# Optimization experiments

Hardware: AMD Instinct MI355X
Metric: run time of the kernel (lower is better)

## Reference

```python
import jax, jax.numpy as jnp
import numpy as np

B, N, C, H = 32, 577, 768, 12

def setup_inputs() -> dict:
    key = jax.random.key(0)
    k1, k2, k3, k4 = jax.random.split(key, 4)
    x = jax.random.normal(k1, (B, N, C), dtype=jnp.float32)
    prev = jax.random.normal(k2, (B, H, N, N), dtype=jnp.float32)
    Wqkv = jax.random.normal(k3, (3 * C, C), dtype=jnp.float32) * (C ** -0.5)
    Wproj = jax.random.normal(k4, (C, C), dtype=jnp.float32) * (C ** -0.5)
    bproj = jnp.zeros((C,), dtype=jnp.float32)
    return {"x": x, "prev": prev, "Wqkv": Wqkv, "Wproj": Wproj, "bproj": bproj}

def reference(x, prev, Wqkv, Wproj, bproj):
    b, n, c = x.shape
    h = H
    hd = c // h
    scale = hd ** -0.5
    # qkv: [B, N, 3C] -> [3, B, H, N, hd]
    qkv = (x @ Wqkv.T).reshape(b, n, 3, h, hd).transpose(2, 0, 3, 1, 4)
    q, k, v = qkv[0], qkv[1], qkv[2]
    # pre-softmax scores with residual passthrough (res_score=True)
    scores = jnp.einsum('bhqd,bhkd->bhqk', q, k) * scale + prev
    attn = jax.nn.softmax(scores, axis=-1)
    out = jnp.einsum('bhqk,bhkd->bhqd', attn, v)  # [B, H, N, hd]
    out = out.transpose(0, 2, 1, 3).reshape(b, n, c)
    out = out @ Wproj.T + bproj
    return out, scores
```

## Files before the change

### kernel.cpp

```cpp
#include <hip/hip_runtime.h>
#include <cstdint>
#include <cstddef>

using short8   = __attribute__((ext_vector_type(8))) short;
using f32x4    = __attribute__((ext_vector_type(4))) float;
using ushort4v = __attribute__((ext_vector_type(4))) unsigned short;

#define B_    32
#define N_    577
#define C_    768
#define H_    12
#define HD_   64
#define NPAD  640
#define MROWS 18464
#define MPAD  18560
#define NQKV  2304
#define SCALE 0.125f
#define OUT0_ELTS 14180352

static __device__ __forceinline__ unsigned short f2bf(float f) {
  union { float f; unsigned int u; } v; v.f = f;
  return (unsigned short)((v.u + 0x7FFFu + ((v.u >> 16) & 1u)) >> 16);
}

static __device__ __forceinline__ void gload_lds16(const unsigned short* g, unsigned short* l) {
  __builtin_amdgcn_global_load_lds(
      (const __attribute__((address_space(1))) unsigned int*)g,
      (__attribute__((address_space(3))) unsigned int*)l, 16, 0, 0);
}

__global__ __launch_bounds__(256) void cvt_f32_bf16(const float* __restrict__ src,
                                                    unsigned short* __restrict__ dst, int n4) {
  int i = blockIdx.x * 256 + threadIdx.x;
  if (i >= n4) return;
  f32x4 v = ((const f32x4*)src)[i];
  ushort4v o;
  o.x = f2bf(v.x); o.y = f2bf(v.y); o.z = f2bf(v.z); o.w = f2bf(v.w);
  ((ushort4v*)dst)[i] = o;
}

__global__ __launch_bounds__(256) void gemm_qkv(
    const unsigned short* __restrict__ A,
    const unsigned short* __restrict__ Bw,
    unsigned short* __restrict__ qb,
    unsigned short* __restrict__ kbuf,
    unsigned short* __restrict__ vtb)
{
  __shared__ unsigned short As[128 * 64];
  __shared__ unsigned short Bs[128 * 64];
  const int mt = blockIdx.x, nt = blockIdx.y;
  const int tid = threadIdx.x;
  const int wave = tid >> 6, lane = tid & 63;
  const int wm = wave >> 1, wn = wave & 1;
  const int lq = lane & 15, grp = lane >> 4;

  f32x4 acc[4][4] = {};

  const int arowbase = mt * 128;
  const int browbase = nt * 128;
  const int srow = wave * 8 + (lane >> 3);
  const int scol = (lane & 7) * 8;

  for (int kblk = 0; kblk < 12; ++kblk) {
    const int koff = kblk * 64;
#pragma unroll
    for (int i = 0; i < 4; ++i) {
      gload_lds16(A  + (size_t)(arowbase + i * 32 + srow) * 768 + koff + scol,
                  &As[(i * 32 + wave * 8) * 64]);
      gload_lds16(Bw + (size_t)(browbase + i * 32 + srow) * 768 + koff + scol,
                  &Bs[(i * 32 + wave * 8) * 64]);
    }
    __syncthreads();
#pragma unroll
    for (int ks = 0; ks < 2; ++ks) {
      short8 af[4], bf[4];
#pragma unroll
      for (int mi = 0; mi < 4; ++mi)
        af[mi] = *(const short8*)&As[(wm * 64 + mi * 16 + lq) * 64 + ks * 32 + grp * 8];
#pragma unroll
      for (int ni = 0; ni < 4; ++ni)
        bf[ni] = *(const short8*)&Bs[(wn * 64 + ni * 16 + lq) * 64 + ks * 32 + grp * 8];
#pragma unroll
      for (int mi = 0; mi < 4; ++mi)
#pragma unroll
        for (int ni = 0; ni < 4; ++ni)
          acc[mi][ni] = __builtin_amdgcn_mfma_f32_16x16x32_bf16(af[mi], bf[ni], acc[mi][ni], 0, 0, 0);
    }
    __syncthreads();
  }

#pragma unroll
  for (int mi = 0; mi < 4; ++mi) {
#pragma unroll
    for (int ni = 0; ni < 4; ++ni) {
      const int n = browbase + wn * 64 + ni * 16 + lq;
      const unsigned s = (unsigned)n / 768u;
      const int rem = n - (int)s * 768;
      const int hh = rem >> 6, d = rem & 63;
#pragma unroll
      for (int j = 0; j < 4; ++j) {
        const int m = arowbase + wm * 64 + mi * 16 + grp * 4 + j;
        if (m < MROWS) {
          const unsigned bb = (unsigned)m / 577u;
          const int t = m - (int)bb * 577;
          const unsigned short bv = f2bf(acc[mi][ni][j]);
          const size_t bh = (size_t)bb * H_ + hh;
          if (s == 0)      qb  [(bh * NPAD + t) * HD_ + d] = bv;
          else if (s == 1) kbuf[(bh * NPAD + t) * HD_ + d] = bv;
          else             vtb [(bh * HD_ + d) * NPAD + t] = bv;
        }
      }
    }
  }
}

__global__ __launch_bounds__(256, 3) void attn_kernel(
    const unsigned short* __restrict__ qb,
    const unsigned short* __restrict__ kb,
    const unsigned short* __restrict__ vtb,
    const float* __restrict__ prev,
    float* __restrict__ scores_out,
    unsigned short* __restrict__ ob)
{
  const int qblk = blockIdx.x;
  const int bh   = blockIdx.y;
  const int wave = threadIdx.x >> 6;
  const int lane = threadIdx.x & 63;
  const int lq = lane & 15, grp = lane >> 4;

  const int b = bh / H_;
  const int h = bh - b * H_;

  const unsigned short* qp = qb  + (size_t)bh * NPAD * HD_;
  const unsigned short* kp = kb  + (size_t)bh * NPAD * HD_;
  const unsigned short* vp = vtb + (size_t)bh * HD_ * NPAD;

  const int qrow = qblk * 64 + wave * 16 + lq;
  const bool qvalid = (qrow < N_);

  const float* prevrow = prev + ((size_t)bh * N_ + qrow) * N_;
  float* srow = scores_out + ((size_t)bh * N_ + qrow) * N_;

  short8 qf0, qf1;
  {
    const unsigned short* qr = qp + (size_t)qrow * HD_ + grp * 8;
    qf0 = *(const short8*)(qr);
    qf1 = *(const short8*)(qr + 32);
  }

  f32x4 oacc[4] = {};
  float lacc = 0.f;

  __shared__ __attribute__((aligned(16))) unsigned short plds[2][4][16][72];

  auto loadK = [&](int kblk, short8 kf[8]) {
#pragma unroll
    for (int t = 0; t < 4; ++t) {
      const unsigned short* kr = kp + (size_t)(kblk * 64 + t * 16 + lq) * HD_ + grp * 8;
      kf[2 * t]     = *(const short8*)(kr);
      kf[2 * t + 1] = *(const short8*)(kr + 32);
    }
  };
  auto loadPrev = [&](int kblk, float pv[16]) {
#pragma unroll
    for (int t = 0; t < 4; ++t) {
      const int kg0 = kblk * 64 + t * 16 + grp * 4;
      float tmp[4] = {0.f, 0.f, 0.f, 0.f};
      if (qvalid) {
        if (kg0 + 3 < N_) {
          __builtin_memcpy(tmp, prevrow + kg0, 16);
        } else {
#pragma unroll
          for (int e = 0; e < 4; ++e)
            if (kg0 + e < N_) tmp[e] = prevrow[kg0 + e];
        }
      }
#pragma unroll
      for (int e = 0; e < 4; ++e) pv[t * 4 + e] = tmp[e];
    }
  };

  short8 kf[8];
  float  pv[16];
  loadK(0, kf);
  loadPrev(0, pv);

  for (int kblk = 0; kblk < 10; ++kblk) {
    const int kbase = kblk * 64;

    short8 vf[8];
#pragma unroll
    for (int dt = 0; dt < 4; ++dt) {
      const unsigned short* vr = vp + (size_t)(dt * 16 + lq) * NPAD + kbase + grp * 8;
      vf[2 * dt]     = *(const short8*)(vr);
      vf[2 * dt + 1] = *(const short8*)(vr + 32);
    }

    float pvn[16];
    if (kblk < 9) loadPrev(kblk + 1, pvn);

    f32x4 sacc[4] = {};
#pragma unroll
    for (int t = 0; t < 4; ++t) {
      sacc[t] = __builtin_amdgcn_mfma_f32_16x16x32_bf16(kf[2 * t],     qf0, sacc[t], 0, 0, 0);
      sacc[t] = __builtin_amdgcn_mfma_f32_16x16x32_bf16(kf[2 * t + 1], qf1, sacc[t], 0, 0, 0);
    }

    short8 kfn[8];
    if (kblk < 9) loadK(kblk + 1, kfn);

    float p[16];
#pragma unroll
    for (int t = 0; t < 4; ++t) {
      const int kg0 = kbase + t * 16 + grp * 4;
      float sv[4];
#pragma unroll
      for (int r = 0; r < 4; ++r) {
        float sval = sacc[t][r] * SCALE + pv[t * 4 + r];
        if (kg0 + r >= N_) sval = -__builtin_inff();
        sv[r] = sval;
        float e = __expf(sval);
        p[t * 4 + r] = e;
        lacc += e;
      }
      if (qvalid) {
        if (kg0 + 3 < N_) {
          __builtin_memcpy(srow + kg0, sv, 16);
        } else {
#pragma unroll
          for (int e2 = 0; e2 < 4; ++e2)
            if (kg0 + e2 < N_) srow[kg0 + e2] = sv[e2];
        }
      }
    }

    const int pb = kblk & 1;
#pragma unroll
    for (int t = 0; t < 4; ++t) {
      ushort4v pw;
      pw.x = f2bf(p[t * 4 + 0]); pw.y = f2bf(p[t * 4 + 1]);
      pw.z = f2bf(p[t * 4 + 2]); pw.w = f2bf(p[t * 4 + 3]);
      *(ushort4v*)(&plds[pb][wave][lq][t * 16 + grp * 4]) = pw;
    }
    short8 pf0 = *(const short8*)(&plds[pb][wave][lq][grp * 8]);
    short8 pf1 = *(const short8*)(&plds[pb][wave][lq][32 + grp * 8]);

#pragma unroll
    for (int dt = 0; dt < 4; ++dt) {
      oacc[dt] = __builtin_amdgcn_mfma_f32_16x16x32_bf16(vf[2 * dt],     pf0, oacc[dt], 0, 0, 0);
      oacc[dt] = __builtin_amdgcn_mfma_f32_16x16x32_bf16(vf[2 * dt + 1], pf1, oacc[dt], 0, 0, 0);
    }

    if (kblk < 9) {
#pragma unroll
      for (int i = 0; i < 16; ++i) pv[i] = pvn[i];
#pragma unroll
      for (int i = 0; i < 8; ++i) kf[i] = kfn[i];
    }
  }

  lacc += __shfl_xor(lacc, 16, 64);
  lacc += __shfl_xor(lacc, 32, 64);

  if (qvalid) {
    const float rl = 1.0f / lacc;
    unsigned short* orow = ob + (size_t)(b * N_ + qrow) * C_ + h * HD_;
#pragma unroll
    for (int dt = 0; dt < 4; ++dt) {
      ushort4v ow;
      ow.x = f2bf(oacc[dt][0] * rl); ow.y = f2bf(oacc[dt][1] * rl);
      ow.z = f2bf(oacc[dt][2] * rl); ow.w = f2bf(oacc[dt][3] * rl);
      *(ushort4v*)(orow + dt * 16 + grp * 4) = ow;
    }
  }
}

__global__ __launch_bounds__(256) void gemm_proj(
    const unsigned short* __restrict__ A,
    const unsigned short* __restrict__ Bw,
    const float* __restrict__ bias,
    float* __restrict__ out0)
{
  __shared__ unsigned short As[128 * 64];
  __shared__ unsigned short Bs[128 * 64];
  const int mt = blockIdx.x, nt = blockIdx.y;
  const int tid = threadIdx.x;
  const int wave = tid >> 6, lane = tid & 63;
  const int wm = wave >> 1, wn = wave & 1;
  const int lq = lane & 15, grp = lane >> 4;

  f32x4 acc[4][4] = {};

  const int arowbase = mt * 128;
  const int browbase = nt * 128;
  const int srow = wave * 8 + (lane >> 3);
  const int scol = (lane & 7) * 8;

  for (int kblk = 0; kblk < 12; ++kblk) {
    const int koff = kblk * 64;
#pragma unroll
    for (int i = 0; i < 4; ++i) {
      gload_lds16(A  + (size_t)(arowbase + i * 32 + srow) * 768 + koff + scol,
                  &As[(i * 32 + wave * 8) * 64]);
      gload_lds16(Bw + (size_t)(browbase + i * 32 + srow) * 768 + koff + scol,
                  &Bs[(i * 32 + wave * 8) * 64]);
    }
    __syncthreads();
#pragma unroll
    for (int ks = 0; ks < 2; ++ks) {
      short8 af[4], bf[4];
#pragma unroll
      for (int mi = 0; mi < 4; ++mi)
        af[mi] = *(const short8*)&As[(wm * 64 + mi * 16 + lq) * 64 + ks * 32 + grp * 8];
#pragma unroll
      for (int ni = 0; ni < 4; ++ni)
        bf[ni] = *(const short8*)&Bs[(wn * 64 + ni * 16 + lq) * 64 + ks * 32 + grp * 8];
#pragma unroll
      for (int mi = 0; mi < 4; ++mi)
#pragma unroll
        for (int ni = 0; ni < 4; ++ni)
          acc[mi][ni] = __builtin_amdgcn_mfma_f32_16x16x32_bf16(af[mi], bf[ni], acc[mi][ni], 0, 0, 0);
    }
    __syncthreads();
  }

#pragma unroll
  for (int ni = 0; ni < 4; ++ni) {
    const int n = browbase + wn * 64 + ni * 16 + lq;
    const float bv = bias[n];
#pragma unroll
    for (int mi = 0; mi < 4; ++mi) {
#pragma unroll
      for (int j = 0; j < 4; ++j) {
        const int m = arowbase + wm * 64 + mi * 16 + grp * 4 + j;
        if (m < MROWS) out0[(size_t)m * C_ + n] = acc[mi][ni][j] + bv;
      }
    }
  }
}

extern "C" void kernel_launch(void* const* d_in, const int* in_sizes, int n_in,
                              void* d_out, int out_size, void* d_ws, size_t ws_size,
                              hipStream_t stream) {
  const float* x     = (const float*)d_in[0];
  const float* prev  = (const float*)d_in[1];
  const float* Wqkv  = (const float*)d_in[2];
  const float* Wproj = (const float*)d_in[3];
  const float* bproj = (const float*)d_in[4];
  float* out = (float*)d_out;

  char* ws = (char*)d_ws;
  size_t off = 0;
  auto alloc = [&](size_t bytes) {
    void* p = ws + off;
    off += (bytes + 255) & ~(size_t)255;
    return p;
  };
  unsigned short* xb     = (unsigned short*)alloc((size_t)MPAD * 768 * 2);
  unsigned short* wqkvb  = (unsigned short*)alloc((size_t)NQKV * 768 * 2);
  unsigned short* wprojb = (unsigned short*)alloc((size_t)768 * 768 * 2);
  unsigned short* qb     = (unsigned short*)alloc((size_t)B_ * H_ * NPAD * HD_ * 2);
  unsigned short* kbuf   = (unsigned short*)alloc((size_t)B_ * H_ * NPAD * HD_ * 2);
  unsigned short* vtb    = (unsigned short*)alloc((size_t)B_ * H_ * HD_ * NPAD * 2);
  unsigned short* ob     = (unsigned short*)alloc((size_t)MPAD * 768 * 2);
  (void)ob;

  hipMemsetAsync(vtb, 0, (size_t)B_ * H_ * HD_ * NPAD * 2, stream);

  {
    int n4 = (B_ * N_ * C_) / 4;
    cvt_f32_bf16<<<(n4 + 255) / 256, 256, 0, stream>>>(x, xb, n4);
    n4 = (NQKV * C_) / 4;
    cvt_f32_bf16<<<(n4 + 255) / 256, 256, 0, stream>>>(Wqkv, wqkvb, n4);
    n4 = (C_ * C_) / 4;
    cvt_f32_bf16<<<(n4 + 255) / 256, 256, 0, stream>>>(Wproj, wprojb, n4);
  }

  gemm_qkv<<<dim3(MPAD / 128, NQKV / 128), 256, 0, stream>>>(xb, wqkvb, qb, kbuf, vtb);

  attn_kernel<<<dim3(10, B_ * H_), 256, 0, stream>>>(qb, kbuf, vtb, prev,
                                                     out + OUT0_ELTS, ob);

  gemm_proj<<<dim3(MPAD / 128, C_ / 128), 256, 0, stream>>>(ob, wprojb, bproj, out);
}
```

Measured before the change: 714.3 us.

## Stage K/V tiles in LDS and coalesce score stores via shared slab

Each K and V tile is now loaded once per block into double-buffered shared memory using direct global-to-LDS loads with an XOR swizzle, instead of every wave fetching its own copy into registers. Scores are written to an LDS slab and read back row-contiguous, so the fp32 score output goes out in coalesced 64-wide row segments. The same slab also rebuilds the P operand layout for the second MFMA, replacing the old bf16 P shuffle buffer. This adds a block-wide barrier per key block and more LDS use, which may reduce occupancy.

```diff
diff --git a/kernel.cpp b/kernel.cpp
--- a/kernel.cpp
+++ b/kernel.cpp
@@ -124,8 +124,9 @@
 {
   const int qblk = blockIdx.x;
   const int bh   = blockIdx.y;
-  const int wave = threadIdx.x >> 6;
-  const int lane = threadIdx.x & 63;
+  const int tid  = threadIdx.x;
+  const int wave = tid >> 6;
+  const int lane = tid & 63;
   const int lq = lane & 15, grp = lane >> 4;
 
   const int b = bh / H_;
@@ -139,7 +140,11 @@
   const bool qvalid = (qrow < N_);
 
   const float* prevrow = prev + ((size_t)bh * N_ + qrow) * N_;
-  float* srow = scores_out + ((size_t)bh * N_ + qrow) * N_;
+  float* srow_base = scores_out + (size_t)bh * N_ * N_;
+
+  __shared__ __attribute__((aligned(16))) unsigned short ldsK[2][4096];
+  __shared__ __attribute__((aligned(16))) unsigned short ldsV[2][4096];
+  __shared__ __attribute__((aligned(16))) float sslab[4][16][68];
 
   short8 qf0, qf1;
   {
@@ -151,16 +156,19 @@
   f32x4 oacc[4] = {};
   float lacc = 0.f;
 
-  __shared__ __attribute__((aligned(16))) unsigned short plds[2][4][16][72];
-
-  auto loadK = [&](int kblk, short8 kf[8]) {
-#pragma unroll
-    for (int t = 0; t < 4; ++t) {
-      const unsigned short* kr = kp + (size_t)(kblk * 64 + t * 16 + lq) * HD_ + grp * 8;
-      kf[2 * t]     = *(const short8*)(kr);
-      kf[2 * t + 1] = *(const short8*)(kr + 32);
+  const int rhi = tid >> 3;
+  const int chk = (tid & 7) ^ (rhi & 7);
+  auto stageKV = [&](int kblk, int bufi) {
+    const int kbase = kblk * 64;
+#pragma unroll
+    for (int r = 0; r < 2; ++r) {
+      gload_lds16(kp + (size_t)(kbase + r * 32 + rhi) * HD_ + chk * 8,
+                  &ldsK[bufi][r * 2048 + wave * 512]);
+      gload_lds16(vp + (size_t)(r * 32 + rhi) * NPAD + kbase + chk * 8,
+                  &ldsV[bufi][r * 2048 + wave * 512]);
     }
   };
+
   auto loadPrev = [&](int kblk, float pv[16]) {
 #pragma unroll
     for (int t = 0; t < 4; ++t) {
@@ -180,82 +188,108 @@
     }
   };
 
-  short8 kf[8];
-  float  pv[16];
-  loadK(0, kf);
+  const int sl0 = ((grp)     ^ (lq & 7)) * 8;
+  const int sl1 = ((grp + 4) ^ (lq & 7)) * 8;
+
+  float pv[16], pvn[16];
+  stageKV(0, 0);
   loadPrev(0, pv);
 
+#pragma unroll 1
   for (int kblk = 0; kblk < 10; ++kblk) {
+    __syncthreads();
+    const int cur = kblk & 1;
     const int kbase = kblk * 64;
 
-    short8 vf[8];
-#pragma unroll
-    for (int dt = 0; dt < 4; ++dt) {
-      const unsigned short* vr = vp + (size_t)(dt * 16 + lq) * NPAD + kbase + grp * 8;
-      vf[2 * dt]     = *(const short8*)(vr);
-      vf[2 * dt + 1] = *(const short8*)(vr + 32);
-    }
-
-    float pvn[16];
-    if (kblk < 9) loadPrev(kblk + 1, pvn);
+    if (kblk < 9) {
+      stageKV(kblk + 1, cur ^ 1);
+      loadPrev(kblk + 1, pvn);
+    }
 
     f32x4 sacc[4] = {};
 #pragma unroll
     for (int t = 0; t < 4; ++t) {
-      sacc[t] = __builtin_amdgcn_mfma_f32_16x16x32_bf16(kf[2 * t],     qf0, sacc[t], 0, 0, 0);
-      sacc[t] = __builtin_amdgcn_mfma_f32_16x16x32_bf16(kf[2 * t + 1], qf1, sacc[t], 0, 0, 0);
-    }
-
-    short8 kfn[8];
-    if (kblk < 9) loadK(kblk + 1, kfn);
-
-    float p[16];
+      const int row = (t * 16 + lq) * 64;
+      short8 a0 = *(const short8*)&ldsK[cur][row + sl0];
+      short8 a1 = *(const short8*)&ldsK[cur][row + sl1];
+      sacc[t] = __builtin_amdgcn_mfma_f32_16x16x32_bf16(a0, qf0, sacc[t], 0, 0, 0);
+      sacc[t] = __builtin_amdgcn_mfma_f32_16x16x32_bf16(a1, qf1, sacc[t], 0, 0, 0);
+    }
+
 #pragma unroll
     for (int t = 0; t < 4; ++t) {
       const int kg0 = kbase + t * 16 + grp * 4;
-      float sv[4];
+      f32x4 sv;
 #pragma unroll
       for (int r = 0; r < 4; ++r) {
         float sval = sacc[t][r] * SCALE + pv[t * 4 + r];
         if (kg0 + r >= N_) sval = -__builtin_inff();
         sv[r] = sval;
-        float e = __expf(sval);
-        p[t * 4 + r] = e;
-        lacc += e;
-      }
-      if (qvalid) {
-        if (kg0 + 3 < N_) {
-          __builtin_memcpy(srow + kg0, sv, 16);
+      }
+      *(f32x4*)&sslab[wave][lq][t * 16 + grp * 4] = sv;
+    }
+
+    short8 pf0, pf1;
+    {
+      const float* sr = &sslab[wave][lq][0];
+      f32x4 x0 = *(const f32x4*)(sr + grp * 8);
+      f32x4 x1 = *(const f32x4*)(sr + grp * 8 + 4);
+      f32x4 x2 = *(const f32x4*)(sr + 32 + grp * 8);
+      f32x4 x3 = *(const f32x4*)(sr + 32 + grp * 8 + 4);
+      float e[16];
+#pragma unroll
+      for (int j = 0; j < 4; ++j) {
+        e[j]      = __expf(x0[j]);
+        e[4 + j]  = __expf(x1[j]);
+        e[8 + j]  = __expf(x2[j]);
+        e[12 + j] = __expf(x3[j]);
+      }
+#pragma unroll
+      for (int j = 0; j < 16; ++j) lacc += e[j];
+      ushort4v pa, pb2, pc, pd;
+#pragma unroll
+      for (int j = 0; j < 4; ++j) {
+        ((unsigned short*)&pa)[j]  = f2bf(e[j]);
+        ((unsigned short*)&pb2)[j] = f2bf(e[4 + j]);
+        ((unsigned short*)&pc)[j]  = f2bf(e[8 + j]);
+        ((unsigned short*)&pd)[j]  = f2bf(e[12 + j]);
+      }
+      union { struct { ushort4v a, b; } s; short8 v; } u0, u1;
+      u0.s.a = pa; u0.s.b = pb2; pf0 = u0.v;
+      u1.s.a = pc; u1.s.b = pd;  pf1 = u1.v;
+    }
+
+#pragma unroll
+    for (int dt = 0; dt < 4; ++dt) {
+      const int row = (dt * 16 + lq) * 64;
+      short8 v0 = *(const short8*)&ldsV[cur][row + sl0];
+      short8 v1 = *(const short8*)&ldsV[cur][row + sl1];
+      oacc[dt] = __builtin_amdgcn_mfma_f32_16x16x32_bf16(v0, pf0, oacc[dt], 0, 0, 0);
+      oacc[dt] = __builtin_amdgcn_mfma_f32_16x16x32_bf16(v1, pf1, oacc[dt], 0, 0, 0);
+    }
+
+#pragma unroll
+    for (int q4 = 0; q4 < 4; ++q4) {
+      const int row16 = q4 * 4 + (lane >> 4);
+      const int qrow_s = qblk * 64 + wave * 16 + row16;
+      const int col0 = (lane & 15) * 4;
+      const int kg = kbase + col0;
+      if (qrow_s < N_) {
+        f32x4 vals = *(const f32x4*)&sslab[wave][row16][col0];
+        float* dst = srow_base + (size_t)qrow_s * N_ + kg;
+        if (kg + 3 < N_) {
+          __builtin_memcpy(dst, &vals, 16);
         } else {
 #pragma unroll
           for (int e2 = 0; e2 < 4; ++e2)
-            if (kg0 + e2 < N_) srow[kg0 + e2] = sv[e2];
+            if (kg + e2 < N_) dst[e2] = vals[e2];
         }
       }
     }
 
-    const int pb = kblk & 1;
-#pragma unroll
-    for (int t = 0; t < 4; ++t) {
-      ushort4v pw;
-      pw.x = f2bf(p[t * 4 + 0]); pw.y = f2bf(p[t * 4 + 1]);
-      pw.z = f2bf(p[t * 4 + 2]); pw.w = f2bf(p[t * 4 + 3]);
-      *(ushort4v*)(&plds[pb][wave][lq][t * 16 + grp * 4]) = pw;
-    }
-    short8 pf0 = *(const short8*)(&plds[pb][wave][lq][grp * 8]);
-    short8 pf1 = *(const short8*)(&plds[pb][wave][lq][32 + grp * 8]);
-
-#pragma unroll
-    for (int dt = 0; dt < 4; ++dt) {
-      oacc[dt] = __builtin_amdgcn_mfma_f32_16x16x32_bf16(vf[2 * dt],     pf0, oacc[dt], 0, 0, 0);
-      oacc[dt] = __builtin_amdgcn_mfma_f32_16x16x32_bf16(vf[2 * dt + 1], pf1, oacc[dt], 0, 0, 0);
-    }
-
     if (kblk < 9) {
 #pragma unroll
       for (int i = 0; i < 16; ++i) pv[i] = pvn[i];
-#pragma unroll
-      for (int i = 0; i < 8; ++i) kf[i] = kfn[i];
     }
   }
 
```

Result: faster. 611.5 us (-14.4%).
